# Optimization experiments

Measured on AMD Instinct MI355X. Metric: run time of the kernel, lower is better.

## Reference

```python
import jax, jax.numpy as jnp
import numpy as np

N_NODES = 100000
N_EDGES = 1600000
IN_FEATS = 256
OUT_FEATS = 128


def setup_inputs() -> dict:
    key = jax.random.key(0)
    k1, k2, k3, k4, k5, k6 = jax.random.split(key, 6)
    feat = jax.random.normal(k1, (N_NODES, IN_FEATS), dtype=jnp.float32)
    # xavier_uniform-style scale for the weight
    limit = float(np.sqrt(6.0 / (IN_FEATS + OUT_FEATS)))
    weight = jax.random.uniform(k2, (IN_FEATS, OUT_FEATS), dtype=jnp.float32, minval=-limit, maxval=limit)
    # degree-normalizer scalars per node (positive, like 1/sqrt(deg))
    cj = jax.random.uniform(k3, (N_NODES, 1), dtype=jnp.float32, minval=0.05, maxval=1.0)
    ci = jax.random.uniform(k4, (N_NODES, 1), dtype=jnp.float32, minval=0.05, maxval=1.0)
    src = jax.random.randint(k5, (N_EDGES,), 0, N_NODES, dtype=jnp.int32)
    dst = jax.random.randint(k6, (N_EDGES,), 0, N_NODES, dtype=jnp.int32)
    return {"feat": feat, "weight": weight, "cj": cj, "ci": ci, "src": src, "dst": dst}


def reference(feat, weight, cj, ci, src, dst):
    # dense transform: [N, in] @ [in, out] -> [N, out]
    h = feat @ weight
    # pre-scale by source normalizer (dropout rate 0 -> identity)
    h = h * cj
    # copy_src + sum aggregation: gather messages at src, scatter-sum into dst
    msgs = h[src]  # [E, out]
    agg = jax.ops.segment_sum(msgs, dst, num_segments=N_NODES)  # [N, out]
    # post-scale by destination normalizer
    return agg * ci
```

## Files before the change

kernel.cpp:

```cpp
#include <hip/hip_runtime.h>

#define N_NODES 100000
#define N_EDGES 1600000
#define IN_F 256
#define OUT_F 128
#define E4 (N_EDGES / 4)

#define BUCKETS 256
#define NPB 391
#define CH 4096
#define NCHUNK ((N_EDGES + CH - 1) / CH)
#define CAP 8192

#define GEMM_T 4
#define GEMM_BLOCKS 196
#define GP_BLOCKS (GEMM_BLOCKS + NCHUNK)

typedef short bf16x8 __attribute__((ext_vector_type(8)));
typedef float f32x4 __attribute__((ext_vector_type(4)));

__device__ __forceinline__ unsigned int f2bf(float f) {
    unsigned int u = __float_as_uint(f);
    return (u + 0x7FFFu + ((u >> 16) & 1u)) >> 16;
}
__device__ __forceinline__ unsigned int pack2(float a, float b) {
    return f2bf(a) | (f2bf(b) << 16);
}
__device__ __forceinline__ float bf_lo(unsigned int u) { return __uint_as_float(u << 16); }
__device__ __forceinline__ float bf_hi(unsigned int u) { return __uint_as_float(u & 0xFFFF0000u); }

__global__ __launch_bounds__(256) void setup_kernel(const float* __restrict__ W,
                                                    unsigned short* __restrict__ Wfrag,
                                                    int* __restrict__ bucket_cursor) {
    int idx = blockIdx.x * 256 + threadIdx.x;
    if (idx < IN_F * OUT_F) {
        int j    = idx & 7;
        int lane = (idx >> 3) & 63;
        int fkt  = idx >> 9;
        int f    = fkt >> 3;
        int kt   = fkt & 7;
        int c    = f * 16 + (lane & 15);
        int k    = kt * 32 + (lane >> 4) * 8 + j;
        Wfrag[idx] = (unsigned short)f2bf(W[k * OUT_F + c]);
    }
    if (blockIdx.x == 0 && threadIdx.x < BUCKETS) bucket_cursor[threadIdx.x] = 0;
}

__global__ __launch_bounds__(512) void gemm_part_kernel(const float* __restrict__ feat,
                                                        const unsigned short* __restrict__ Wfrag,
                                                        const float* __restrict__ cj,
                                                        unsigned short* __restrict__ h,
                                                        const int* __restrict__ src,
                                                        const int* __restrict__ dst,
                                                        int* __restrict__ bucket_cursor,
                                                        uint2* __restrict__ slab) {
    __shared__ __align__(16) char pool[65536 + 8 * 16 * 136 * 2];

    const int bid = blockIdx.x;
    const int tid = threadIdx.x;

    if (bid >= GEMM_BLOCKS) {
        int* hist   = (int*)pool;
        int* hstart = hist + 256;
        int* gbase  = hstart + 256;
        uint2* stage = (uint2*)(pool + 3072);

        const int cb = bid - GEMM_BLOCKS;
        const int e0 = cb * CH;
        int nE = N_EDGES - e0;
        if (nE > CH) nE = CH;

        if (tid < 256) hist[tid] = 0;
        __syncthreads();

        int dv[8], rk[8];
        const int4* d4 = reinterpret_cast<const int4*>(dst);
        #pragma unroll
        for (int i = 0; i < 2; ++i) {
            int li = tid + i * 512;
            int g4 = (e0 >> 2) + li;
            if (li * 4 < nE && g4 < E4) {
                int4 d = d4[g4];
                dv[i*4+0] = d.x; dv[i*4+1] = d.y; dv[i*4+2] = d.z; dv[i*4+3] = d.w;
                rk[i*4+0] = atomicAdd(&hist[d.x / NPB], 1);
                rk[i*4+1] = atomicAdd(&hist[d.y / NPB], 1);
                rk[i*4+2] = atomicAdd(&hist[d.z / NPB], 1);
                rk[i*4+3] = atomicAdd(&hist[d.w / NPB], 1);
            } else {
                dv[i*4+0] = -1; dv[i*4+1] = -1; dv[i*4+2] = -1; dv[i*4+3] = -1;
            }
        }
        __syncthreads();

        int v = 0;
        if (tid < 256) { v = hist[tid]; hstart[tid] = v; }
        __syncthreads();
        #pragma unroll
        for (int off = 1; off < 256; off <<= 1) {
            int u = 0;
            if (tid < 256 && tid >= off) u = hstart[tid - off];
            __syncthreads();
            if (tid < 256) hstart[tid] += u;
            __syncthreads();
        }
        if (tid < 256) {
            int ex = hstart[tid] - v;
            if (v > 0) gbase[tid] = atomicAdd(&bucket_cursor[tid], v);
            hstart[tid] = ex;
        }
        __syncthreads();

        const int4* s4 = reinterpret_cast<const int4*>(src);
        #pragma unroll
        for (int i = 0; i < 2; ++i) {
            int li = tid + i * 512;
            int g4 = (e0 >> 2) + li;
            if (dv[i*4] >= 0) {
                int4 s = s4[g4];
                stage[hstart[dv[i*4+0] / NPB] + rk[i*4+0]] = make_uint2((unsigned)dv[i*4+0], (unsigned)s.x);
                stage[hstart[dv[i*4+1] / NPB] + rk[i*4+1]] = make_uint2((unsigned)dv[i*4+1], (unsigned)s.y);
                stage[hstart[dv[i*4+2] / NPB] + rk[i*4+2]] = make_uint2((unsigned)dv[i*4+2], (unsigned)s.z);
                stage[hstart[dv[i*4+3] / NPB] + rk[i*4+3]] = make_uint2((unsigned)dv[i*4+3], (unsigned)s.w);
            }
        }
        __syncthreads();

        for (int idx = tid; idx < nE; idx += 512) {
            uint2 p = stage[idx];
            int b = (int)p.x / NPB;
            slab[(size_t)b * CAP + gbase[b] + (idx - hstart[b])] = p;
        }
        return;
    }

    unsigned short* wl = (unsigned short*)pool;
    const int wave = tid >> 6;
    const int lane = tid & 63;
    const int r  = lane & 15;
    const int kq = lane >> 4;
    unsigned short* wout = (unsigned short*)(pool + 65536) + wave * (16 * 136);

    float4 fv[16];
    {
        int arow = bid * 512 + wave * 16 + r;
        if (arow >= N_NODES) arow = N_NODES - 1;
        const float4* fr4 = reinterpret_cast<const float4*>(feat + (size_t)arow * IN_F);
        #pragma unroll
        for (int kt = 0; kt < 8; ++kt) {
            fv[2 * kt]     = fr4[kt * 8 + kq * 2];
            fv[2 * kt + 1] = fr4[kt * 8 + kq * 2 + 1];
        }
    }

    {
        const uint4* wsrc = reinterpret_cast<const uint4*>(Wfrag);
        uint4* wdst = reinterpret_cast<uint4*>(wl);
        #pragma unroll
        for (int i = 0; i < 8; ++i) wdst[tid + i * 512] = wsrc[tid + i * 512];
    }
    __syncthreads();

    for (int t = 0; t < GEMM_T; ++t) {
        const int rowbase = bid * 512 + t * 128 + wave * 16;

        bf16x8 a[8];
        #pragma unroll
        for (int kt = 0; kt < 8; ++kt) {
            uint4 au;
            au.x = pack2(fv[2 * kt].x,     fv[2 * kt].y);
            au.y = pack2(fv[2 * kt].z,     fv[2 * kt].w);
            au.z = pack2(fv[2 * kt + 1].x, fv[2 * kt + 1].y);
            au.w = pack2(fv[2 * kt + 1].z, fv[2 * kt + 1].w);
            a[kt] = *reinterpret_cast<bf16x8*>(&au);
        }

        if (t < GEMM_T - 1) {
            int arow = bid * 512 + (t + 1) * 128 + wave * 16 + r;
            if (arow >= N_NODES) arow = N_NODES - 1;
            const float4* fr4 = reinterpret_cast<const float4*>(feat + (size_t)arow * IN_F);
            #pragma unroll
            for (int kt = 0; kt < 8; ++kt) {
                fv[2 * kt]     = fr4[kt * 8 + kq * 2];
                fv[2 * kt + 1] = fr4[kt * 8 + kq * 2 + 1];
            }
        }

        f32x4 acc[8];
        #pragma unroll
        for (int f = 0; f < 8; ++f) acc[f] = (f32x4){0.f, 0.f, 0.f, 0.f};

        #pragma unroll
        for (int kt = 0; kt < 8; ++kt) {
            #pragma unroll
            for (int f = 0; f < 8; ++f) {
                bf16x8 b = *reinterpret_cast<const bf16x8*>(&wl[((f * 8 + kt) * 64 + lane) * 8]);
                acc[f] = __builtin_amdgcn_mfma_f32_16x16x32_bf16(a[kt], b, acc[f], 0, 0, 0);
            }
        }

        int orow[4]; float cjv[4];
        #pragma unroll
        for (int i = 0; i < 4; ++i) {
            orow[i] = rowbase + kq * 4 + i;
            cjv[i] = cj[orow[i] < N_NODES ? orow[i] : 0];
        }

        #pragma unroll
        for (int f = 0; f < 8; ++f) {
            #pragma unroll
            for (int i = 0; i < 4; ++i) {
                wout[(kq * 4 + i) * 136 + f * 16 + r] =
                    (unsigned short)f2bf(acc[f][i] * cjv[i]);
            }
        }
        __syncthreads();

        {
            int row = lane >> 2;
            int ch  = lane & 3;
            int grow = rowbase + row;
            if (grow < N_NODES) {
                uint4* hv = reinterpret_cast<uint4*>(h);
                #pragma unroll
                for (int j = 0; j < 4; ++j) {
                    uint4 vv = *reinterpret_cast<const uint4*>(
                        (const char*)wout + row * 272 + (ch + 4 * j) * 16);
                    hv[(size_t)grow * 16 + ch + 4 * j] = vv;
                }
            }
        }
        __syncthreads();
    }
}

__global__ __launch_bounds__(256) void bin_kernel(const uint2* __restrict__ slab,
                                                  const int* __restrict__ bucket_cursor,
                                                  int* __restrict__ offsets,
                                                  int* __restrict__ bin_src) {
    __shared__ int hist[392];
    __shared__ int cur[392];
    __shared__ int sbuf[256];
    __shared__ int gb_sh, sz_sh;

    const int b = blockIdx.x;
    const int t = threadIdx.x;
    const int nlo = b * NPB;
    int nn = N_NODES - nlo;
    if (nn > NPB) nn = NPB;

    int v = bucket_cursor[t];
    sbuf[t] = v;
    __syncthreads();
    #pragma unroll
    for (int off = 1; off < 256; off <<= 1) {
        int u = (t >= off) ? sbuf[t - off] : 0;
        __syncthreads();
        sbuf[t] += u;
        __syncthreads();
    }
    if (t == b) { gb_sh = sbuf[t] - v; sz_sh = v; }
    if (b == 0 && t == 0) offsets[N_NODES] = N_EDGES;
    __syncthreads();
    const int gb = gb_sh;
    const int sz = sz_sh;
    const uint2* sl = slab + (size_t)b * CAP;

    for (int j = t; j < 392; j += 256) hist[j] = 0;
    __syncthreads();

    for (int i = t; i < sz; i += 256) atomicAdd(&hist[(int)sl[i].x - nlo], 1);
    __syncthreads();

    int a0 = 0, a1 = 0;
    if (t < 196) { a0 = hist[2 * t]; a1 = hist[2 * t + 1]; }
    int part = a0 + a1;
    sbuf[t] = part;
    __syncthreads();
    #pragma unroll
    for (int off = 1; off < 256; off <<= 1) {
        int u = (t >= off) ? sbuf[t - off] : 0;
        __syncthreads();
        sbuf[t] += u;
        __syncthreads();
    }
    int ex = sbuf[t] - part;
    if (t < 196) {
        int o0 = gb + ex;
        int o1 = o0 + a0;
        if (2 * t < nn)     { offsets[nlo + 2 * t]     = o0; cur[2 * t]     = o0; }
        if (2 * t + 1 < nn) { offsets[nlo + 2 * t + 1] = o1; cur[2 * t + 1] = o1; }
    }
    __syncthreads();

    for (int i = t; i < sz; i += 256) {
        uint2 p = sl[i];
        int pos = atomicAdd(&cur[(int)p.x - nlo], 1);
        bin_src[pos] = (int)p.y;
    }
}

__global__ __launch_bounds__(256) void gather_kernel(const uint4* __restrict__ h4,
                                                     const float* __restrict__ ci,
                                                     const int* __restrict__ offsets,
                                                     const int* __restrict__ bin_src,
                                                     float* __restrict__ out) {
    int node = blockIdx.x * 16 + (threadIdx.x >> 4);
    int lane = threadIdx.x & 15;
    if (node >= N_NODES) return;

    int beg = offsets[node];
    int end = offsets[node + 1];

    float acc[8] = {};
    int i = beg;
    for (; i + 4 <= end; i += 4) {
        int s0 = bin_src[i + 0];
        int s1 = bin_src[i + 1];
        int s2 = bin_src[i + 2];
        int s3 = bin_src[i + 3];
        uint4 v0 = h4[(size_t)s0 * 16 + lane];
        uint4 v1 = h4[(size_t)s1 * 16 + lane];
        uint4 v2 = h4[(size_t)s2 * 16 + lane];
        uint4 v3 = h4[(size_t)s3 * 16 + lane];
        acc[0] += (bf_lo(v0.x) + bf_lo(v1.x)) + (bf_lo(v2.x) + bf_lo(v3.x));
        acc[1] += (bf_hi(v0.x) + bf_hi(v1.x)) + (bf_hi(v2.x) + bf_hi(v3.x));
        acc[2] += (bf_lo(v0.y) + bf_lo(v1.y)) + (bf_lo(v2.y) + bf_lo(v3.y));
        acc[3] += (bf_hi(v0.y) + bf_hi(v1.y)) + (bf_hi(v2.y) + bf_hi(v3.y));
        acc[4] += (bf_lo(v0.z) + bf_lo(v1.z)) + (bf_lo(v2.z) + bf_lo(v3.z));
        acc[5] += (bf_hi(v0.z) + bf_hi(v1.z)) + (bf_hi(v2.z) + bf_hi(v3.z));
        acc[6] += (bf_lo(v0.w) + bf_lo(v1.w)) + (bf_lo(v2.w) + bf_lo(v3.w));
        acc[7] += (bf_hi(v0.w) + bf_hi(v1.w)) + (bf_hi(v2.w) + bf_hi(v3.w));
    }
    for (; i < end; ++i) {
        int s = bin_src[i];
        uint4 v = h4[(size_t)s * 16 + lane];
        acc[0] += bf_lo(v.x); acc[1] += bf_hi(v.x);
        acc[2] += bf_lo(v.y); acc[3] += bf_hi(v.y);
        acc[4] += bf_lo(v.z); acc[5] += bf_hi(v.z);
        acc[6] += bf_lo(v.w); acc[7] += bf_hi(v.w);
    }
    float sc = ci[node];
    float4 o0 = make_float4(acc[0] * sc, acc[1] * sc, acc[2] * sc, acc[3] * sc);
    float4 o1 = make_float4(acc[4] * sc, acc[5] * sc, acc[6] * sc, acc[7] * sc);
    float4* o4 = reinterpret_cast<float4*>(out) + (size_t)node * 32 + lane * 2;
    o4[0] = o0;
    o4[1] = o1;
}

extern "C" void kernel_launch(void* const* d_in, const int* in_sizes, int n_in,
                              void* d_out, int out_size, void* d_ws, size_t ws_size,
                              hipStream_t stream) {
    const float* feat = (const float*)d_in[0];
    const float* W    = (const float*)d_in[1];
    const float* cj   = (const float*)d_in[2];
    const float* ci   = (const float*)d_in[3];
    const int*   src  = (const int*)d_in[4];
    const int*   dst  = (const int*)d_in[5];
    float* out = (float*)d_out;

    const size_t H_BYTES   = (size_t)N_NODES * OUT_F * 2;
    const size_t WT_BYTES  = (size_t)IN_F * OUT_F * 2;
    const size_t OFF_BYTES = (((size_t)(N_NODES + 1) * 4) + 15) & ~(size_t)15;
    const size_t BC_BYTES  = (((size_t)BUCKETS * 4) + 15) & ~(size_t)15;
    const size_t SLAB_BYTES = (size_t)BUCKETS * CAP * 8;

    char* ws = (char*)d_ws;
    unsigned short* h     = (unsigned short*)ws;  ws += H_BYTES;
    unsigned short* Wfrag = (unsigned short*)ws;  ws += WT_BYTES;
    int* offsets        = (int*)ws;   ws += OFF_BYTES;
    int* bucket_cursor  = (int*)ws;   ws += BC_BYTES;
    uint2* slab         = (uint2*)ws; ws += SLAB_BYTES;
    int* bin_src        = (int*)ws;

    setup_kernel<<<128, 256, 0, stream>>>(W, Wfrag, bucket_cursor);

    gemm_part_kernel<<<GP_BLOCKS, 512, 0, stream>>>(feat, Wfrag, cj, h, src, dst,
                                                    bucket_cursor, slab);

    bin_kernel<<<BUCKETS, 256, 0, stream>>>(slab, bucket_cursor, offsets, bin_src);

    gather_kernel<<<(N_NODES + 15) / 16, 256, 0, stream>>>((const uint4*)h, ci, offsets, bin_src, out);
}
```

Baseline: 124.8 us.

## Regroup kernels: fuse W prep into partition, co-run GEMM with per-bucket binning

Edge partitioning moves into its own kernel, which also converts the weight into MFMA fragment layout and now handles 8192 edges per block. The GEMM is then fused with the per-bucket binning pass, so GEMM blocks and bin blocks run concurrently in one launch instead of binning waiting on the GEMM. The bucket cursor is cleared with a memset instead of a setup kernel. The intent is to cut a kernel launch and hide the binning work behind the GEMM, at the cost of making the GEMM wait for partitioning to finish.

```diff
diff --git a/kernel.cpp b/kernel.cpp
--- a/kernel.cpp
+++ b/kernel.cpp
@@ -8,13 +8,13 @@
 
 #define BUCKETS 256
 #define NPB 391
-#define CH 4096
+#define CH 8192
 #define NCHUNK ((N_EDGES + CH - 1) / CH)
 #define CAP 8192
 
 #define GEMM_T 4
 #define GEMM_BLOCKS 196
-#define GP_BLOCKS (GEMM_BLOCKS + NCHUNK)
+#define GB_BLOCKS (GEMM_BLOCKS + BUCKETS)
 
 typedef short bf16x8 __attribute__((ext_vector_type(8)));
 typedef float f32x4 __attribute__((ext_vector_type(4)));
@@ -29,11 +29,22 @@
 __device__ __forceinline__ float bf_lo(unsigned int u) { return __uint_as_float(u << 16); }
 __device__ __forceinline__ float bf_hi(unsigned int u) { return __uint_as_float(u & 0xFFFF0000u); }
 
-__global__ __launch_bounds__(256) void setup_kernel(const float* __restrict__ W,
-                                                    unsigned short* __restrict__ Wfrag,
-                                                    int* __restrict__ bucket_cursor) {
-    int idx = blockIdx.x * 256 + threadIdx.x;
-    if (idx < IN_F * OUT_F) {
+__global__ __launch_bounds__(512) void part_kernel(const float* __restrict__ W,
+                                                   unsigned short* __restrict__ Wfrag,
+                                                   const int* __restrict__ src,
+                                                   const int* __restrict__ dst,
+                                                   int* __restrict__ bucket_cursor,
+                                                   uint2* __restrict__ slab) {
+    __shared__ int hist[256];
+    __shared__ int hstart[256];
+    __shared__ int gbase[256];
+    __shared__ uint2 stage[CH];
+
+    const int bid = blockIdx.x;
+    const int t = threadIdx.x;
+
+    if (bid < 64) {
+        int idx = bid * 512 + t;
         int j    = idx & 7;
         int lane = (idx >> 3) & 63;
         int fkt  = idx >> 9;
@@ -43,92 +54,141 @@
         int k    = kt * 32 + (lane >> 4) * 8 + j;
         Wfrag[idx] = (unsigned short)f2bf(W[k * OUT_F + c]);
     }
-    if (blockIdx.x == 0 && threadIdx.x < BUCKETS) bucket_cursor[threadIdx.x] = 0;
-}
-
-__global__ __launch_bounds__(512) void gemm_part_kernel(const float* __restrict__ feat,
-                                                        const unsigned short* __restrict__ Wfrag,
-                                                        const float* __restrict__ cj,
-                                                        unsigned short* __restrict__ h,
-                                                        const int* __restrict__ src,
-                                                        const int* __restrict__ dst,
-                                                        int* __restrict__ bucket_cursor,
-                                                        uint2* __restrict__ slab) {
+
+    const int e0 = bid * CH;
+    int nE = N_EDGES - e0;
+    if (nE > CH) nE = CH;
+
+    if (t < 256) hist[t] = 0;
+    __syncthreads();
+
+    int dv[16], rk[16];
+    const int4* d4 = reinterpret_cast<const int4*>(dst);
+    #pragma unroll
+    for (int i = 0; i < 4; ++i) {
+        int li = t + i * 512;
+        int g4 = (e0 >> 2) + li;
+        if (li * 4 < nE && g4 < E4) {
+            int4 d = d4[g4];
+            dv[i*4+0] = d.x; dv[i*4+1] = d.y; dv[i*4+2] = d.z; dv[i*4+3] = d.w;
+            rk[i*4+0] = atomicAdd(&hist[d.x / NPB], 1);
+            rk[i*4+1] = atomicAdd(&hist[d.y / NPB], 1);
+            rk[i*4+2] = atomicAdd(&hist[d.z / NPB], 1);
+            rk[i*4+3] = atomicAdd(&hist[d.w / NPB], 1);
+        } else {
+            dv[i*4+0] = -1; dv[i*4+1] = -1; dv[i*4+2] = -1; dv[i*4+3] = -1;
+        }
+    }
+    __syncthreads();
+
+    int v = 0;
+    if (t < 256) { v = hist[t]; hstart[t] = v; }
+    __syncthreads();
+    #pragma unroll
+    for (int off = 1; off < 256; off <<= 1) {
+        int u = 0;
+        if (t < 256 && t >= off) u = hstart[t - off];
+        __syncthreads();
+        if (t < 256) hstart[t] += u;
+        __syncthreads();
+    }
+    if (t < 256) {
+        int ex = hstart[t] - v;
+        if (v > 0) gbase[t] = atomicAdd(&bucket_cursor[t], v);
+        hstart[t] = ex;
+    }
+    __syncthreads();
+
+    const int4* s4 = reinterpret_cast<const int4*>(src);
+    #pragma unroll
+    for (int i = 0; i < 4; ++i) {
+        int li = t + i * 512;
+        int g4 = (e0 >> 2) + li;
+        if (dv[i*4] >= 0) {
+            int4 s = s4[g4];
+            stage[hstart[dv[i*4+0] / NPB] + rk[i*4+0]] = make_uint2((unsigned)dv[i*4+0], (unsigned)s.x);
+            stage[hstart[dv[i*4+1] / NPB] + rk[i*4+1]] = make_uint2((unsigned)dv[i*4+1], (unsigned)s.y);
+            stage[hstart[dv[i*4+2] / NPB] + rk[i*4+2]] = make_uint2((unsigned)dv[i*4+2], (unsigned)s.z);
+            stage[hstart[dv[i*4+3] / NPB] + rk[i*4+3]] = make_uint2((unsigned)dv[i*4+3], (unsigned)s.w);
+        }
+    }
+    __syncthreads();
+
+    for (int idx = t; idx < nE; idx += 512) {
+        uint2 p = stage[idx];
+        int b = (int)p.x / NPB;
+        slab[(size_t)b * CAP + gbase[b] + (idx - hstart[b])] = p;
+    }
+}
+
+__global__ __launch_bounds__(512) void gemm_bin_kernel(const float* __restrict__ feat,
+                                                       const unsigned short* __restrict__ Wfrag,
+                                                       const float* __restrict__ cj,
+                                                       unsigned short* __restrict__ h,
+                                                       const uint2* __restrict__ slab,
+                                                       const int* __restrict__ bucket_cursor,
+                                                       int* __restrict__ offsets,
+                                                       int* __restrict__ bin_src) {
     __shared__ __align__(16) char pool[65536 + 8 * 16 * 136 * 2];
 
     const int bid = blockIdx.x;
     const int tid = threadIdx.x;
 
     if (bid >= GEMM_BLOCKS) {
-        int* hist   = (int*)pool;
-        int* hstart = hist + 256;
-        int* gbase  = hstart + 256;
-        uint2* stage = (uint2*)(pool + 3072);
-
-        const int cb = bid - GEMM_BLOCKS;
-        const int e0 = cb * CH;
-        int nE = N_EDGES - e0;
-        if (nE > CH) nE = CH;
-
-        if (tid < 256) hist[tid] = 0;
-        __syncthreads();
-
-        int dv[8], rk[8];
-        const int4* d4 = reinterpret_cast<const int4*>(dst);
-        #pragma unroll
-        for (int i = 0; i < 2; ++i) {
-            int li = tid + i * 512;
-            int g4 = (e0 >> 2) + li;
-            if (li * 4 < nE && g4 < E4) {
-                int4 d = d4[g4];
-                dv[i*4+0] = d.x; dv[i*4+1] = d.y; dv[i*4+2] = d.z; dv[i*4+3] = d.w;
-                rk[i*4+0] = atomicAdd(&hist[d.x / NPB], 1);
-                rk[i*4+1] = atomicAdd(&hist[d.y / NPB], 1);
-                rk[i*4+2] = atomicAdd(&hist[d.z / NPB], 1);
-                rk[i*4+3] = atomicAdd(&hist[d.w / NPB], 1);
-            } else {
-                dv[i*4+0] = -1; dv[i*4+1] = -1; dv[i*4+2] = -1; dv[i*4+3] = -1;
-            }
-        }
-        __syncthreads();
-
-        int v = 0;
-        if (tid < 256) { v = hist[tid]; hstart[tid] = v; }
-        __syncthreads();
-        #pragma unroll
-        for (int off = 1; off < 256; off <<= 1) {
-            int u = 0;
-            if (tid < 256 && tid >= off) u = hstart[tid - off];
+        int* hist = (int*)pool;
+        int* cur  = hist + 392;
+        int* sbuf = cur + 392;
+        int* gbsz = sbuf + 512;
+
+        const int b = bid - GEMM_BLOCKS;
+        const int nlo = b * NPB;
+        int nn = N_NODES - nlo;
+        if (nn > NPB) nn = NPB;
+
+        int v = (tid < 256) ? bucket_cursor[tid] : 0;
+        sbuf[tid] = v;
+        __syncthreads();
+        #pragma unroll
+        for (int off = 1; off < 512; off <<= 1) {
+            int u = (tid >= off) ? sbuf[tid - off] : 0;
             __syncthreads();
-            if (tid < 256) hstart[tid] += u;
+            sbuf[tid] += u;
             __syncthreads();
         }
-        if (tid < 256) {
-            int ex = hstart[tid] - v;
-            if (v > 0) gbase[tid] = atomicAdd(&bucket_cursor[tid], v);
-            hstart[tid] = ex;
-        }
-        __syncthreads();
-
-        const int4* s4 = reinterpret_cast<const int4*>(src);
-        #pragma unroll
-        for (int i = 0; i < 2; ++i) {
-            int li = tid + i * 512;
-            int g4 = (e0 >> 2) + li;
-            if (dv[i*4] >= 0) {
-                int4 s = s4[g4];
-                stage[hstart[dv[i*4+0] / NPB] + rk[i*4+0]] = make_uint2((unsigned)dv[i*4+0], (unsigned)s.x);
-                stage[hstart[dv[i*4+1] / NPB] + rk[i*4+1]] = make_uint2((unsigned)dv[i*4+1], (unsigned)s.y);
-                stage[hstart[dv[i*4+2] / NPB] + rk[i*4+2]] = make_uint2((unsigned)dv[i*4+2], (unsigned)s.z);
-                stage[hstart[dv[i*4+3] / NPB] + rk[i*4+3]] = make_uint2((unsigned)dv[i*4+3], (unsigned)s.w);
-            }
-        }
-        __syncthreads();
-
-        for (int idx = tid; idx < nE; idx += 512) {
-            uint2 p = stage[idx];
-            int b = (int)p.x / NPB;
-            slab[(size_t)b * CAP + gbase[b] + (idx - hstart[b])] = p;
+        if (tid == b) { gbsz[0] = sbuf[tid] - v; gbsz[1] = v; }
+        if (b == 0 && tid == 0) offsets[N_NODES] = N_EDGES;
+        __syncthreads();
+        const int gb = gbsz[0];
+        const int sz = gbsz[1];
+        const uint2* sl = slab + (size_t)b * CAP;
+
+        for (int j = tid; j < 392; j += 512) hist[j] = 0;
+        __syncthreads();
+
+        for (int i = tid; i < sz; i += 512) atomicAdd(&hist[(int)sl[i].x - nlo], 1);
+        __syncthreads();
+
+        int hv = (tid < 391) ? hist[tid] : 0;
+        sbuf[tid] = hv;
+        __syncthreads();
+        #pragma unroll
+        for (int off = 1; off < 512; off <<= 1) {
+            int u = (tid >= off) ? sbuf[tid - off] : 0;
+            __syncthreads();
+            sbuf[tid] += u;
+            __syncthreads();
+        }
+        if (tid < nn) {
+            int o = gb + sbuf[tid] - hv;
+            offsets[nlo + tid] = o;
+            cur[tid] = o;
+        }
+        __syncthreads();
+
+        for (int i = tid; i < sz; i += 512) {
+            uint2 p = sl[i];
+            int pos = atomicAdd(&cur[(int)p.x - nlo], 1);
+            bin_src[pos] = (int)p.y;
         }
         return;
     }
@@ -230,72 +290,6 @@
             }
         }
         __syncthreads();
-    }
-}
-
-__global__ __launch_bounds__(256) void bin_kernel(const uint2* __restrict__ slab,
-                                                  const int* __restrict__ bucket_cursor,
-                                                  int* __restrict__ offsets,
-                                                  int* __restrict__ bin_src) {
-    __shared__ int hist[392];
-    __shared__ int cur[392];
-    __shared__ int sbuf[256];
-    __shared__ int gb_sh, sz_sh;
-
-    const int b = blockIdx.x;
-    const int t = threadIdx.x;
-    const int nlo = b * NPB;
-    int nn = N_NODES - nlo;
-    if (nn > NPB) nn = NPB;
-
-    int v = bucket_cursor[t];
-    sbuf[t] = v;
-    __syncthreads();
-    #pragma unroll
-    for (int off = 1; off < 256; off <<= 1) {
-        int u = (t >= off) ? sbuf[t - off] : 0;
-        __syncthreads();
-        sbuf[t] += u;
-        __syncthreads();
-    }
-    if (t == b) { gb_sh = sbuf[t] - v; sz_sh = v; }
-    if (b == 0 && t == 0) offsets[N_NODES] = N_EDGES;
-    __syncthreads();
-    const int gb = gb_sh;
-    const int sz = sz_sh;
-    const uint2* sl = slab + (size_t)b * CAP;
-
-    for (int j = t; j < 392; j += 256) hist[j] = 0;
-    __syncthreads();
-
-    for (int i = t; i < sz; i += 256) atomicAdd(&hist[(int)sl[i].x - nlo], 1);
-    __syncthreads();
-
-    int a0 = 0, a1 = 0;
-    if (t < 196) { a0 = hist[2 * t]; a1 = hist[2 * t + 1]; }
-    int part = a0 + a1;
-    sbuf[t] = part;
-    __syncthreads();
-    #pragma unroll
-    for (int off = 1; off < 256; off <<= 1) {
-        int u = (t >= off) ? sbuf[t - off] : 0;
-        __syncthreads();
-        sbuf[t] += u;
-        __syncthreads();
-    }
-    int ex = sbuf[t] - part;
-    if (t < 196) {
-        int o0 = gb + ex;
-        int o1 = o0 + a0;
-        if (2 * t < nn)     { offsets[nlo + 2 * t]     = o0; cur[2 * t]     = o0; }
-        if (2 * t + 1 < nn) { offsets[nlo + 2 * t + 1] = o1; cur[2 * t + 1] = o1; }
-    }
-    __syncthreads();
-
-    for (int i = t; i < sz; i += 256) {
-        uint2 p = sl[i];
-        int pos = atomicAdd(&cur[(int)p.x - nlo], 1);
-        bin_src[pos] = (int)p.y;
     }
 }
 
@@ -372,12 +366,12 @@
     uint2* slab         = (uint2*)ws; ws += SLAB_BYTES;
     int* bin_src        = (int*)ws;
 
-    setup_kernel<<<128, 256, 0, stream>>>(W, Wfrag, bucket_cursor);
-
-    gemm_part_kernel<<<GP_BLOCKS, 512, 0, stream>>>(feat, Wfrag, cj, h, src, dst,
-                                                    bucket_cursor, slab);
-
-    bin_kernel<<<BUCKETS, 256, 0, stream>>>(slab, bucket_cursor, offsets, bin_src);
+    hipMemsetAsync(bucket_cursor, 0, (size_t)BUCKETS * 4, stream);
+
+    part_kernel<<<NCHUNK, 512, 0, stream>>>(W, Wfrag, src, dst, bucket_cursor, slab);
+
+    gemm_bin_kernel<<<GB_BLOCKS, 512, 0, stream>>>(feat, Wfrag, cj, h, slab,
+                                                   bucket_cursor, offsets, bin_src);
 
     gather_kernel<<<(N_NODES + 15) / 16, 256, 0, stream>>>((const uint4*)h, ci, offsets, bin_src, out);
 }
```

Measured after the change: 123.6 us. Within noise of the previous version (-1.0%).
